# Optimization experiments

Measured on AMD Instinct MI355X. Metric: run time of the kernel, lower is better.

Reference implementation:

```python
import jax, jax.numpy as jnp
import numpy as np

EPS = 1e-12  # F.normalize default eps


def setup_inputs() -> dict:
    key = jax.random.key(0)
    k1, k2, k3 = jax.random.split(key, 3)
    B, C, H, W = 4, 64, 64, 64
    background = jax.random.normal(k1, (B, C, H, W), dtype=jnp.float32)
    foreground = jax.random.normal(k2, (B, C, H, W), dtype=jnp.float32)
    # binary mask, broadcast over channels
    mask = jnp.round(jax.random.uniform(k3, (B, 1, H, W), dtype=jnp.float32))
    return {"background": background, "foreground": foreground, "mask": mask}


def _l2norm(x, axis):
    # matches torch F.normalize: x / max(||x||, eps)
    n = jnp.sqrt(jnp.sum(x * x, axis=axis, keepdims=True))
    return x / jnp.maximum(n, EPS)


def reference(background, foreground, mask):
    B, C, H, W = background.shape
    bg_flat = background.reshape(B, C, H * W)   # [B, C, K]
    fg_flat = foreground.reshape(B, C, H * W)   # [B, C, Q]
    norm_bg = _l2norm(bg_flat, axis=1)
    norm_fg = _l2norm(fg_flat, axis=1)
    # cosine-similarity scores [B, K, Q]
    attention = jnp.einsum('bck,bcq->bkq', norm_bg, norm_fg)
    attention = jax.nn.softmax(attention, axis=1)  # over bg (key) axis
    attended = jnp.einsum('bck,bkq->bcq', bg_flat, attention)
    attended = attended.reshape(B, C, H, W)
    return foreground * (1.0 - mask) + attended * mask
```

## Files before the change

### kernel.cpp

```cpp
#include <hip/hip_runtime.h>
#include <math.h>

#define CC 64
#define HWN 4096
#define QB 64
#define KSPLIT 8
#define KT 32
#define NITER (HWN / KSPLIT / KT)
#define NKC (HWN / KT)

typedef __attribute__((ext_vector_type(8))) short bf16x8;
typedef __attribute__((ext_vector_type(4))) float f32x4;

__device__ __align__(16) unsigned short g_bgT[4][HWN][CC];
__device__ __align__(16) unsigned short g_bgN[4][NKC][CC][KT];
__device__ __align__(16) unsigned short g_fgT[4][HWN][CC];

static __device__ __forceinline__ unsigned int f2bf(float x) {
  union { float f; unsigned int u; } v; v.f = x;
  return (v.u + 0x7fffu + ((v.u >> 16) & 1u)) >> 16;
}
static __device__ __forceinline__ unsigned int packbf(float lo, float hi) {
  return f2bf(lo) | (f2bf(hi) << 16);
}

__global__ __launch_bounds__(256) void prep_kernel(const float* __restrict__ bg,
                                                   const float* __restrict__ fg) {
  __shared__ float lds[32 * 65];
  const int bid = blockIdx.x;
  const int kc = bid & 127, b = (bid >> 7) & 3, which = bid >> 9;
  const float* src = (which ? fg : bg) + (size_t)b * CC * HWN + kc * KT;
  const int tid = threadIdx.x;

  {
    int c = tid >> 2, k0 = (tid & 3) * 8;
#pragma unroll
    for (int j4 = 0; j4 < 2; ++j4) {
      float4 v = *(const float4*)(src + (size_t)c * HWN + k0 + 4 * j4);
      lds[(k0 + 4 * j4 + 0) * 65 + c] = v.x;
      lds[(k0 + 4 * j4 + 1) * 65 + c] = v.y;
      lds[(k0 + 4 * j4 + 2) * 65 + c] = v.z;
      lds[(k0 + 4 * j4 + 3) * 65 + c] = v.w;
    }
  }
  __syncthreads();

  const int k = tid >> 3, u = tid & 7;
  float ss = 0.f;
#pragma unroll
  for (int j = 0; j < 8; ++j) {
    float v = lds[k * 65 + u * 8 + j];
    ss = fmaf(v, v, ss);
  }
  ss += __shfl_xor(ss, 1, 64);
  ss += __shfl_xor(ss, 2, 64);
  ss += __shfl_xor(ss, 4, 64);
  const float s = 1.0f / fmaxf(sqrtf(ss), 1e-12f);

  {
    unsigned int* gT32 = (unsigned int*)(which ? &g_fgT[0][0][0] : &g_bgT[0][0][0]);
    size_t R = (size_t)b * HWN + kc * KT + k;
    unsigned int w4[4];
#pragma unroll
    for (int i = 0; i < 4; ++i) {
      int c2 = u * 8 + 2 * i;
      w4[i] = packbf(lds[k * 65 + c2] * s, lds[k * 65 + c2 + 1] * s);
    }
    *(uint4*)&gT32[R * 32 + u * 4] = make_uint4(w4[0], w4[1], w4[2], w4[3]);
  }

  if (which == 0) {
    unsigned int* gN32 = (unsigned int*)&g_bgN[0][0][0][0];
    int cN = tid >> 2, vN = tid & 3;
    unsigned int n4[4];
#pragma unroll
    for (int i = 0; i < 4; ++i) {
      int kk = vN * 8 + 2 * i;
      n4[i] = packbf(lds[kk * 65 + cN], lds[(kk + 1) * 65 + cN]);
    }
    size_t RN = (((size_t)b * NKC + kc) * CC + cN) * (KT / 2) + vN * 4;
    *(uint4*)&gN32[RN] = make_uint4(n4[0], n4[1], n4[2], n4[3]);
  }
}

#define P_OFF 65536
#define ML_OFF 106496
#define SMEM_BYTES 108544
__global__ __launch_bounds__(512, 2) void attn_kernel(const float* __restrict__ fg,
                                                      const float* __restrict__ mask,
                                                      float* __restrict__ out) {
  __shared__ __align__(16) char smem[SMEM_BYTES];
  const int wg = blockIdx.x;
  const int wgp = (wg & 7) * 32 + (wg >> 3);
  const int b = wgp >> 6;
  const int q0 = (wgp & 63) * QB;
  const int tid = threadIdx.x;
  const int lane = tid & 63;
  const int ks = tid >> 6;
  const int m16 = lane & 15;
  const int quad = lane >> 4;

  bf16x8 Bf[4][2];
#pragma unroll
  for (int qf = 0; qf < 4; ++qf)
#pragma unroll
    for (int h = 0; h < 2; ++h)
      Bf[qf][h] = *(const bf16x8*)&g_fgT[b][q0 + qf * 16 + m16][h * 32 + quad * 8];

  const unsigned short* srcT[4];
#pragma unroll
  for (int t = 0; t < 4; ++t) {
    int uT = t * 64 + lane;
    int kk = uT >> 3, pos = uT & 7, j = pos ^ (kk & 7);
    srcT[t] = &g_bgT[b][ks * 512 + kk][j * 8];
  }

  const unsigned short* pN = &g_bgN[b][ks * 16][m16][quad * 8];

  unsigned short* P = (unsigned short*)(smem + P_OFF + ks * 5120);
  float* mL = (float*)(smem + ML_OFF);

  float l_run[4] = {0.f, 0.f, 0.f, 0.f};
  f32x4 O[4][4];
#pragma unroll
  for (int t = 0; t < 4; ++t)
#pragma unroll
    for (int qf = 0; qf < 4; ++qf) O[t][qf] = (f32x4){0.f, 0.f, 0.f, 0.f};

  char* const myT = smem + ks * 8192;

  auto stageT = [&](int bufsel) {
#pragma unroll
    for (int t = 0; t < 4; ++t) {
      __builtin_amdgcn_global_load_lds(
          (const __attribute__((address_space(1))) unsigned int*)srcT[t],
          (__attribute__((address_space(3))) unsigned int*)(myT + bufsel * 4096 + t * 1024),
          16, 0, 0);
      srcT[t] += KT * CC;
    }
  };

  bf16x8 A0r[4], A1r[4];
  auto loadN = [&](bf16x8 (&A)[4], int ch) {
#pragma unroll
    for (int t = 0; t < 4; ++t)
      A[t] = *(const bf16x8*)(pN + (size_t)ch * (CC * KT) + t * 16 * KT);
  };

  auto iter = [&](int it, int co, bf16x8 (&Ac)[4], bf16x8 (&An)[4]) {
    if (it + 1 < NITER) {
      stageT(co ^ 1);
      loadN(An, it + 1);
      asm volatile("s_waitcnt vmcnt(8)" ::: "memory");
    } else {
      asm volatile("s_waitcnt vmcnt(0)" ::: "memory");
    }

    const char* baseT = myT + co * 4096;

    f32x4 S[4][2];
    __builtin_amdgcn_s_setprio(1);
#pragma unroll
    for (int i = 0; i < 2; ++i) {
      int kk = 16 * i + m16;
      bf16x8 T0 = *(const bf16x8*)(baseT + kk * 128 + ((quad) ^ (kk & 7)) * 16);
      bf16x8 T1 = *(const bf16x8*)(baseT + kk * 128 + ((4 + quad) ^ (kk & 7)) * 16);
#pragma unroll
      for (int qf = 0; qf < 4; ++qf) {
        f32x4 acc = {0.f, 0.f, 0.f, 0.f};
        acc = __builtin_amdgcn_mfma_f32_16x16x32_bf16(T0, Bf[qf][0], acc, 0, 0, 0);
        acc = __builtin_amdgcn_mfma_f32_16x16x32_bf16(T1, Bf[qf][1], acc, 0, 0, 0);
        S[qf][i] = acc;
      }
    }
    __builtin_amdgcn_s_setprio(0);

#pragma unroll
    for (int qf = 0; qf < 4; ++qf)
#pragma unroll
      for (int i = 0; i < 2; ++i) {
        float pe[4];
#pragma unroll
        for (int r = 0; r < 4; ++r) {
          pe[r] = __expf(S[qf][i][r] - 1.0f);
          l_run[qf] += pe[r];
        }
        union { float f; unsigned int u; } x0, x1, x2, x3;
        x0.f = pe[0]; x1.f = pe[1]; x2.f = pe[2]; x3.f = pe[3];
        unsigned int p01 = __builtin_amdgcn_perm(x1.u + 0x8000u, x0.u + 0x8000u, 0x07060302u);
        unsigned int p23 = __builtin_amdgcn_perm(x3.u + 0x8000u, x2.u + 0x8000u, 0x07060302u);
        *(uint2*)&P[(qf * 16 + m16) * 40 + 16 * i + quad * 4] = make_uint2(p01, p23);
      }

    bf16x8 Pf[4];
#pragma unroll
    for (int qf = 0; qf < 4; ++qf)
      Pf[qf] = *(const bf16x8*)&P[(qf * 16 + m16) * 40 + quad * 8];
    __builtin_amdgcn_s_setprio(1);
#pragma unroll
    for (int t = 0; t < 4; ++t)
#pragma unroll
      for (int qf = 0; qf < 4; ++qf)
        O[t][qf] = __builtin_amdgcn_mfma_f32_16x16x32_bf16(Ac[t], Pf[qf], O[t][qf], 0, 0, 0);
    __builtin_amdgcn_s_setprio(0);
  };

  stageT(0);
  loadN(A0r, 0);

  for (int it2 = 0; it2 < NITER; it2 += 2) {
    iter(it2,     0, A0r, A1r);
    iter(it2 + 1, 1, A1r, A0r);
  }

#pragma unroll
  for (int qf = 0; qf < 4; ++qf) {
    l_run[qf] += __shfl_xor(l_run[qf], 16, 64);
    l_run[qf] += __shfl_xor(l_run[qf], 32, 64);
  }
  if (quad == 0) {
#pragma unroll
    for (int qf = 0; qf < 4; ++qf) mL[ks * 64 + qf * 16 + m16] = l_run[qf];
  }
  float* mO = (float*)smem;
  const float* fgB = fg + (size_t)b * CC * HWN;
  const float* mk = mask + (size_t)b * HWN;
  float* outB = out + (size_t)b * CC * HWN;

#pragma unroll
  for (int half = 0; half < 2; ++half) {
    __syncthreads();
#pragma unroll
    for (int qh = 0; qh < 2; ++qh) {
      int qf = half * 2 + qh;
#pragma unroll
      for (int t = 0; t < 4; ++t)
#pragma unroll
        for (int r = 0; r < 4; ++r)
          mO[(ks * 64 + 16 * t + quad * 4 + r) * 34 + qh * 16 + m16] = O[t][qf][r];
    }
    __syncthreads();
    {
      int q = tid & 31, cb = tid >> 5;
      int qglob = q0 + half * 32 + q;
      float L = 0.f;
#pragma unroll
      for (int s = 0; s < 8; ++s) L += mL[s * 64 + half * 32 + q];
      float invL = 1.0f / L;
      float mv = mk[qglob];
#pragma unroll
      for (int e = 0; e < 4; ++e) {
        int c = cb * 4 + e;
        float acc = 0.f;
#pragma unroll
        for (int s = 0; s < 8; ++s) acc += mO[(s * 64 + c) * 34 + q];
        float att = acc * invL;
        float fgv = fgB[(size_t)c * HWN + qglob];
        outB[(size_t)c * HWN + qglob] = fgv + mv * (att - fgv);
      }
    }
  }
}

extern "C" void kernel_launch(void* const* d_in, const int* in_sizes, int n_in,
                              void* d_out, int out_size, void* d_ws, size_t ws_size,
                              hipStream_t stream) {
  const float* background = (const float*)d_in[0];
  const float* foreground = (const float*)d_in[1];
  const float* mask       = (const float*)d_in[2];
  float* out = (float*)d_out;
  prep_kernel<<<1024, 256, 0, stream>>>(background, foreground);
  attn_kernel<<<dim3(HWN / QB * 4), 512, 0, stream>>>(foreground, mask, out);
}
```

Measured before the change: 92.08 us.

## Fuse prep and attention into one cooperative kernel with grid sync

```diff
diff --git a/kernel.cpp b/kernel.cpp
--- a/kernel.cpp
+++ b/kernel.cpp
@@ -1,5 +1,8 @@
 #include <hip/hip_runtime.h>
+#include <hip/hip_cooperative_groups.h>
 #include <math.h>
+
+namespace cg = cooperative_groups;
 
 #define CC 64
 #define HWN 4096
@@ -24,77 +27,85 @@
   return f2bf(lo) | (f2bf(hi) << 16);
 }
 
-__global__ __launch_bounds__(256) void prep_kernel(const float* __restrict__ bg,
-                                                   const float* __restrict__ fg) {
-  __shared__ float lds[32 * 65];
-  const int bid = blockIdx.x;
-  const int kc = bid & 127, b = (bid >> 7) & 3, which = bid >> 9;
-  const float* src = (which ? fg : bg) + (size_t)b * CC * HWN + kc * KT;
-  const int tid = threadIdx.x;
-
-  {
-    int c = tid >> 2, k0 = (tid & 3) * 8;
-#pragma unroll
-    for (int j4 = 0; j4 < 2; ++j4) {
-      float4 v = *(const float4*)(src + (size_t)c * HWN + k0 + 4 * j4);
-      lds[(k0 + 4 * j4 + 0) * 65 + c] = v.x;
-      lds[(k0 + 4 * j4 + 1) * 65 + c] = v.y;
-      lds[(k0 + 4 * j4 + 2) * 65 + c] = v.z;
-      lds[(k0 + 4 * j4 + 3) * 65 + c] = v.w;
-    }
-  }
-  __syncthreads();
-
-  const int k = tid >> 3, u = tid & 7;
-  float ss = 0.f;
-#pragma unroll
-  for (int j = 0; j < 8; ++j) {
-    float v = lds[k * 65 + u * 8 + j];
-    ss = fmaf(v, v, ss);
-  }
-  ss += __shfl_xor(ss, 1, 64);
-  ss += __shfl_xor(ss, 2, 64);
-  ss += __shfl_xor(ss, 4, 64);
-  const float s = 1.0f / fmaxf(sqrtf(ss), 1e-12f);
-
-  {
-    unsigned int* gT32 = (unsigned int*)(which ? &g_fgT[0][0][0] : &g_bgT[0][0][0]);
-    size_t R = (size_t)b * HWN + kc * KT + k;
-    unsigned int w4[4];
-#pragma unroll
-    for (int i = 0; i < 4; ++i) {
-      int c2 = u * 8 + 2 * i;
-      w4[i] = packbf(lds[k * 65 + c2] * s, lds[k * 65 + c2 + 1] * s);
-    }
-    *(uint4*)&gT32[R * 32 + u * 4] = make_uint4(w4[0], w4[1], w4[2], w4[3]);
-  }
-
-  if (which == 0) {
-    unsigned int* gN32 = (unsigned int*)&g_bgN[0][0][0][0];
-    int cN = tid >> 2, vN = tid & 3;
-    unsigned int n4[4];
-#pragma unroll
-    for (int i = 0; i < 4; ++i) {
-      int kk = vN * 8 + 2 * i;
-      n4[i] = packbf(lds[kk * 65 + cN], lds[(kk + 1) * 65 + cN]);
-    }
-    size_t RN = (((size_t)b * NKC + kc) * CC + cN) * (KT / 2) + vN * 4;
-    *(uint4*)&gN32[RN] = make_uint4(n4[0], n4[1], n4[2], n4[3]);
-  }
-}
-
 #define P_OFF 65536
 #define ML_OFF 106496
 #define SMEM_BYTES 108544
-__global__ __launch_bounds__(512, 2) void attn_kernel(const float* __restrict__ fg,
-                                                      const float* __restrict__ mask,
-                                                      float* __restrict__ out) {
+__global__ __launch_bounds__(512, 2) void fused_kernel(const float* __restrict__ bg,
+                                                       const float* __restrict__ fgin,
+                                                       const float* __restrict__ mask,
+                                                       float* __restrict__ out) {
   __shared__ __align__(16) char smem[SMEM_BYTES];
+  const int tid = threadIdx.x;
   const int wg = blockIdx.x;
+
+  {
+    float* plds = (float*)smem + (tid >> 8) * (32 * 65);
+    const int t256 = tid & 255;
+#pragma unroll
+    for (int round = 0; round < 2; ++round) {
+      const int tile = wg * 4 + round * 2 + (tid >> 8);
+      const int kc = tile & 127, bb = (tile >> 7) & 3, which = tile >> 9;
+      const float* src = (which ? fgin : bg) + (size_t)bb * CC * HWN + kc * KT;
+
+      {
+        int c = t256 >> 2, k0 = (t256 & 3) * 8;
+#pragma unroll
+        for (int j4 = 0; j4 < 2; ++j4) {
+          float4 v = *(const float4*)(src + (size_t)c * HWN + k0 + 4 * j4);
+          plds[(k0 + 4 * j4 + 0) * 65 + c] = v.x;
+          plds[(k0 + 4 * j4 + 1) * 65 + c] = v.y;
+          plds[(k0 + 4 * j4 + 2) * 65 + c] = v.z;
+          plds[(k0 + 4 * j4 + 3) * 65 + c] = v.w;
+        }
+      }
+      __syncthreads();
+
+      const int k = t256 >> 3, u = t256 & 7;
+      float ss = 0.f;
+#pragma unroll
+      for (int j = 0; j < 8; ++j) {
+        float v = plds[k * 65 + u * 8 + j];
+        ss = fmaf(v, v, ss);
+      }
+      ss += __shfl_xor(ss, 1, 64);
+      ss += __shfl_xor(ss, 2, 64);
+      ss += __shfl_xor(ss, 4, 64);
+      const float s = 1.0f / fmaxf(sqrtf(ss), 1e-12f);
+
+      {
+        unsigned int* gT32 = (unsigned int*)(which ? &g_fgT[0][0][0] : &g_bgT[0][0][0]);
+        size_t R = (size_t)bb * HWN + kc * KT + k;
+        unsigned int w4[4];
+#pragma unroll
+        for (int i = 0; i < 4; ++i) {
+          int c2 = u * 8 + 2 * i;
+          w4[i] = packbf(plds[k * 65 + c2] * s, plds[k * 65 + c2 + 1] * s);
+        }
+        *(uint4*)&gT32[R * 32 + u * 4] = make_uint4(w4[0], w4[1], w4[2], w4[3]);
+      }
+
+      if (which == 0) {
+        unsigned int* gN32 = (unsigned int*)&g_bgN[0][0][0][0];
+        int cN = t256 >> 2, vN = t256 & 3;
+        unsigned int n4[4];
+#pragma unroll
+        for (int i = 0; i < 4; ++i) {
+          int kk = vN * 8 + 2 * i;
+          n4[i] = packbf(plds[kk * 65 + cN], plds[(kk + 1) * 65 + cN]);
+        }
+        size_t RN = (((size_t)bb * NKC + kc) * CC + cN) * (KT / 2) + vN * 4;
+        *(uint4*)&gN32[RN] = make_uint4(n4[0], n4[1], n4[2], n4[3]);
+      }
+      __syncthreads();
+    }
+  }
+
+  __threadfence();
+  cg::this_grid().sync();
+
   const int wgp = (wg & 7) * 32 + (wg >> 3);
   const int b = wgp >> 6;
   const int q0 = (wgp & 63) * QB;
-  const int tid = threadIdx.x;
   const int lane = tid & 63;
   const int ks = tid >> 6;
   const int m16 = lane & 15;
@@ -223,7 +234,7 @@
     for (int qf = 0; qf < 4; ++qf) mL[ks * 64 + qf * 16 + m16] = l_run[qf];
   }
   float* mO = (float*)smem;
-  const float* fgB = fg + (size_t)b * CC * HWN;
+  const float* fgB = fgin + (size_t)b * CC * HWN;
   const float* mk = mask + (size_t)b * HWN;
   float* outB = out + (size_t)b * CC * HWN;
 
@@ -269,6 +280,6 @@
   const float* foreground = (const float*)d_in[1];
   const float* mask       = (const float*)d_in[2];
   float* out = (float*)d_out;
-  prep_kernel<<<1024, 256, 0, stream>>>(background, foreground);
-  attn_kernel<<<dim3(HWN / QB * 4), 512, 0, stream>>>(foreground, mask, out);
-}
+  void* args[] = {(void*)&background, (void*)&foreground, (void*)&mask, (void*)&out};
+  hipLaunchCooperativeKernel((void*)fused_kernel, dim3(256), dim3(512), args, 0, stream);
+}
```

New measurement: 185.1 us. 101% more time.
